# Optimization experiments

Measured on AMD Instinct MI355X. Metric: run time of the kernel, lower is better.

Reference implementation:

```python
import jax, jax.numpy as jnp
import numpy as np

N_NODES = 100000
N_EDGES = 1600000
IN_SIZE = 128
HIDDEN = 32
OUT_SIZE = 16


def _mean_agg(h, src, dst, n_nodes):
    # segment-sum of source features into destination nodes, then divide by in-degree
    summed = jax.ops.segment_sum(h[src], dst, num_segments=n_nodes)  # [N, D]
    deg = jax.ops.segment_sum(jnp.ones((src.shape[0],), h.dtype), dst, num_segments=n_nodes)
    return summed / jnp.maximum(deg, 1.0)[:, None]


def _sage_layer(h, src, dst, W_self, W_neigh, b):
    # DGL SAGEConv (mean): fc_self(h) + fc_neigh(mean_neigh(h)) + bias
    agg = _mean_agg(h, src, dst, h.shape[0])
    return h @ W_self + agg @ W_neigh + b


def setup_inputs() -> dict:
    key = jax.random.key(0)
    ks = jax.random.split(key, 9)
    inp = {
        "x": jax.random.normal(ks[0], (N_NODES, IN_SIZE), jnp.float32),
        "edge_src": jax.random.randint(ks[1], (N_EDGES,), 0, N_NODES, jnp.int32),
        "edge_dst": jax.random.randint(ks[2], (N_EDGES,), 0, N_NODES, jnp.int32),
        "W_self1": jax.random.normal(ks[3], (IN_SIZE, HIDDEN), jnp.float32) / np.sqrt(IN_SIZE),
        "W_neigh1": jax.random.normal(ks[4], (IN_SIZE, HIDDEN), jnp.float32) / np.sqrt(IN_SIZE),
        "b1": jnp.zeros((HIDDEN,), jnp.float32),
        "W_self2": jax.random.normal(ks[5], (HIDDEN, HIDDEN), jnp.float32) / np.sqrt(HIDDEN),
        "W_neigh2": jax.random.normal(ks[6], (HIDDEN, HIDDEN), jnp.float32) / np.sqrt(HIDDEN),
        "b2": jnp.zeros((HIDDEN,), jnp.float32),
        "W_self3": jax.random.normal(ks[7], (HIDDEN, OUT_SIZE), jnp.float32) / np.sqrt(HIDDEN),
        "W_neigh3": jax.random.normal(ks[8], (HIDDEN, OUT_SIZE), jnp.float32) / np.sqrt(HIDDEN),
        "b3": jnp.zeros((OUT_SIZE,), jnp.float32),
    }
    return inp


def reference(x, edge_src, edge_dst,
              W_self1, W_neigh1, b1,
              W_self2, W_neigh2, b2,
              W_self3, W_neigh3, b3):
    h = jax.nn.relu(_sage_layer(x, edge_src, edge_dst, W_self1, W_neigh1, b1))
    h = jax.nn.relu(_sage_layer(h, edge_src, edge_dst, W_self2, W_neigh2, b2))
    h = _sage_layer(h, edge_src, edge_dst, W_self3, W_neigh3, b3)
    return h
```

## Files before the change

kernel.cpp:

```cpp
#include <hip/hip_runtime.h>


#define BLOCK 256
#define NBLK 256
#define BSH 9
#define CAP 12288

typedef __attribute__((ext_vector_type(8))) short bf16x8;
typedef __attribute__((ext_vector_type(4))) float f32x4;

__device__ __forceinline__ unsigned pack_bf16(float a, float b) {
    unsigned ua = __float_as_uint(a); ua = (ua + 0x7fffu + ((ua >> 16) & 1u)) >> 16;
    unsigned ub = __float_as_uint(b); ub = (ub + 0x7fffu + ((ub >> 16) & 1u)) >> 16;
    return ua | (ub << 16);
}
__device__ __forceinline__ unsigned short bf16r(float f) {
    unsigned u = __float_as_uint(f);
    return (unsigned short)((u + 0x7fffu + ((u >> 16) & 1u)) >> 16);
}
__device__ __forceinline__ float bf2f(unsigned short u) {
    return __uint_as_float((unsigned)u << 16);
}

__global__ void prep_kernel(const float* __restrict__ Ws1, const float* __restrict__ Wn1,
                            const float* __restrict__ Ws2, const float* __restrict__ Wn2,
                            const float* __restrict__ Ws3, const float* __restrict__ Wn3,
                            unsigned short* __restrict__ Wt1,
                            unsigned short* __restrict__ Wt2,
                            unsigned short* __restrict__ Wt3) {
    int stride = gridDim.x * BLOCK;
    int t0 = blockIdx.x * BLOCK + threadIdx.x;
    for (int i = t0; i < 64 * 128; i += stride) {
        int o = i / 128, k = i % 128;
        float v = (o < 32) ? Ws1[k * 32 + o] : Wn1[k * 32 + (o - 32)];
        Wt1[i] = bf16r(v);
    }
    for (int i = t0; i < 64 * 32; i += stride) {
        int o = i / 32, k = i % 32;
        float v = (o < 32) ? Ws2[k * 32 + o] : Wn2[k * 32 + (o - 32)];
        Wt2[i] = bf16r(v);
    }
    for (int i = t0; i < 32 * 32; i += stride) {
        int o = i / 32, k = i % 32;
        float v = (o < 16) ? Ws3[k * 16 + o] : Wn3[k * 16 + (o - 16)];
        Wt3[i] = bf16r(v);
    }
}

__global__ __launch_bounds__(256, 4)
void stage1_kernel(const int* __restrict__ dst, int* __restrict__ hist,
                   int n_edges, int nbuk, int ch,
                   const float* __restrict__ x,
                   const unsigned short* __restrict__ Wt,
                   const float* __restrict__ bias,
                   unsigned short* __restrict__ pre,
                   unsigned short* __restrict__ p,
                   int n_nodes, int nHist) {
    __shared__ int cnt[256];
    int bid = blockIdx.x;
    int tid = threadIdx.x;

    if (bid < nHist) {
        for (int i = tid; i < nbuk; i += BLOCK) cnt[i] = 0;
        __syncthreads();
        int e0 = bid * ch;
        int e1 = e0 + ch; if (e1 > n_edges) e1 = n_edges;
        for (int e = e0 + tid; e < e1; e += BLOCK)
            atomicAdd(&cnt[dst[e] >> BSH], 1);
        __syncthreads();
        for (int i = tid; i < nbuk; i += BLOCK)
            hist[i * NBLK + bid] = cnt[i];
        return;
    }

    int pb = bid - nHist;
    int wv = tid >> 6, l = tid & 63;
    int col = l & 15, kg = l >> 4;
    int node0 = pb * 64 + wv * 16;

    int arow = node0 + col;
    if (arow >= n_nodes) arow = n_nodes - 1;
    const float* xr = x + (size_t)arow * 128 + kg * 8;

    f32x4 acc[4];
#pragma unroll
    for (int t = 0; t < 4; ++t) acc[t] = (f32x4){0.f, 0.f, 0.f, 0.f};

#pragma unroll
    for (int ks = 0; ks < 4; ++ks) {
        float4 f0 = *reinterpret_cast<const float4*>(xr + ks * 32);
        float4 f1 = *reinterpret_cast<const float4*>(xr + ks * 32 + 4);
        union { bf16x8 v; unsigned u[4]; } A;
        A.u[0] = pack_bf16(f0.x, f0.y);
        A.u[1] = pack_bf16(f0.z, f0.w);
        A.u[2] = pack_bf16(f1.x, f1.y);
        A.u[3] = pack_bf16(f1.z, f1.w);
#pragma unroll
        for (int t = 0; t < 4; ++t) {
            bf16x8 B = *reinterpret_cast<const bf16x8*>(
                Wt + (size_t)(t * 16 + col) * 128 + ks * 32 + kg * 8);
            acc[t] = __builtin_amdgcn_mfma_f32_16x16x32_bf16(A.v, B, acc[t], 0, 0, 0);
        }
    }

    int nodeb = node0 + kg * 4;
#pragma unroll
    for (int t = 0; t < 4; ++t) {
        int out = t * 16 + col;
#pragma unroll
        for (int r = 0; r < 4; ++r) {
            int node = nodeb + r;
            if (node >= n_nodes) continue;
            if (t < 2) {
                pre[(size_t)node * 32 + out] = bf16r(acc[t][r] + bias[out]);
            } else {
                p[(size_t)node * 32 + (out - 32)] = bf16r(acc[t][r]);
            }
        }
    }
}

__global__ void scanBlk_kernel(int* __restrict__ hist, int* __restrict__ buktot) {
    int b = blockIdx.x;
    int tid = threadIdx.x;
    int orig = hist[b * NBLK + tid];
    int v = orig;
    int lane = tid & 63, w = tid >> 6;
#pragma unroll
    for (int off = 1; off < 64; off <<= 1) {
        int u = __shfl_up(v, off);
        if (lane >= off) v += u;
    }
    __shared__ int wps[4];
    if (lane == 63) wps[w] = v;
    __syncthreads();
    int wadd = 0;
    for (int k = 0; k < w; ++k) wadd += wps[k];
    int excl = v - orig + wadd;
    hist[b * NBLK + tid] = excl;
    if (tid == 255) buktot[b] = excl + orig;
}

__global__ void scanBuk_kernel(const int* __restrict__ buktot, int* __restrict__ bukoff,
                               int nbuk, int* __restrict__ startp, int n_nodes, int n_edges) {
    int tid = threadIdx.x;
    int orig = (tid < nbuk) ? buktot[tid] : 0;
    int v = orig;
    int lane = tid & 63, w = tid >> 6;
#pragma unroll
    for (int off = 1; off < 64; off <<= 1) {
        int u = __shfl_up(v, off);
        if (lane >= off) v += u;
    }
    __shared__ int wps[4];
    if (lane == 63) wps[w] = v;
    __syncthreads();
    int wadd = 0;
    for (int k = 0; k < w; ++k) wadd += wps[k];
    int excl = v - orig + wadd;
    if (tid < nbuk) bukoff[tid] = excl;
    if (tid == 0) { bukoff[nbuk] = n_edges; startp[n_nodes] = n_edges; }
}

__global__ void part_kernel(const int* __restrict__ src, const int* __restrict__ dst,
                            const int* __restrict__ hist, const int* __restrict__ bukoff,
                            unsigned* __restrict__ pairs, int n_edges, int nbuk, int ch) {
    __shared__ int base[256];
    __shared__ int cnt[256];
    int tid = threadIdx.x;
    for (int i = tid; i < nbuk; i += BLOCK) {
        base[i] = hist[i * NBLK + blockIdx.x] + bukoff[i];
        cnt[i] = 0;
    }
    __syncthreads();
    int e0 = blockIdx.x * ch;
    int e1 = e0 + ch; if (e1 > n_edges) e1 = n_edges;
    for (int e = e0 + tid; e < e1; e += BLOCK) {
        int d = dst[e];
        int b = d >> BSH;
        unsigned dl = (unsigned)(d & ((1 << BSH) - 1));
        int r = atomicAdd(&cnt[b], 1);
        pairs[base[b] + r] = (unsigned)src[e] | (dl << 20);
    }
}

__global__ void build_kernel(const unsigned* __restrict__ pairs, const int* __restrict__ bukoff,
                             int* __restrict__ start, float* __restrict__ invdeg,
                             int* __restrict__ csr_src, int n_nodes) {
    __shared__ int deg[512];
    __shared__ int lst[512];
    __shared__ int cur[512];
    __shared__ int wps[4];
    __shared__ int scsr[CAP];

    int b = blockIdx.x;
    int tid = threadIdx.x;
    int e0 = bukoff[b];
    int e1 = bukoff[b + 1];
    int lo = b << BSH;
    int hi = lo + (1 << BSH); if (hi > n_nodes) hi = n_nodes;
    int nn = hi - lo;
    int ne = e1 - e0;

    for (int i = tid; i < 512; i += BLOCK) deg[i] = 0;
    __syncthreads();
    for (int i = e0 + tid; i < e1; i += BLOCK)
        atomicAdd(&deg[pairs[i] >> 20], 1);
    __syncthreads();

    int d0 = deg[2 * tid], d1 = deg[2 * tid + 1];
    int s = d0 + d1;
    int lane = tid & 63, w = tid >> 6;
    int v = s;
#pragma unroll
    for (int off = 1; off < 64; off <<= 1) {
        int u = __shfl_up(v, off);
        if (lane >= off) v += u;
    }
    if (lane == 63) wps[w] = v;
    __syncthreads();
    int wb = 0;
    for (int k = 0; k < w; ++k) wb += wps[k];
    int excl = wb + v - s;
    lst[2 * tid] = excl;
    lst[2 * tid + 1] = excl + d0;
    cur[2 * tid] = 0;
    cur[2 * tid + 1] = 0;
    __syncthreads();

    for (int i = tid; i < nn; i += BLOCK) {
        start[lo + i] = e0 + lst[i];
        int d = deg[i];
        invdeg[lo + i] = 1.0f / (float)(d < 1 ? 1 : d);
    }

    if (ne <= CAP) {
        for (int i = e0 + tid; i < e1; i += BLOCK) {
            unsigned pr = pairs[i];
            int dl = pr >> 20;
            int sl = lst[dl] + atomicAdd(&cur[dl], 1);
            scsr[sl] = (int)(pr & 0xFFFFFu);
        }
        __syncthreads();
        for (int i = tid; i < ne; i += BLOCK) csr_src[e0 + i] = scsr[i];
    } else {
        for (int i = e0 + tid; i < e1; i += BLOCK) {
            unsigned pr = pairs[i];
            int dl = pr >> 20;
            int sl = lst[dl] + atomicAdd(&cur[dl], 1);
            csr_src[e0 + sl] = (int)(pr & 0xFFFFFu);
        }
    }
}

template<int DOUT>
__global__ __launch_bounds__(256, 4)
void proj23_mfma(const unsigned short* __restrict__ h,
                 const unsigned short* __restrict__ Wt,
                 const float* __restrict__ bias,
                 unsigned short* __restrict__ pre,
                 unsigned short* __restrict__ p,
                 int n_nodes) {
    constexpr int NTILE = DOUT / 8;
    int tid = threadIdx.x;
    int wv = tid >> 6, l = tid & 63;
    int col = l & 15, kg = l >> 4;
    int node0 = blockIdx.x * 64 + wv * 16;

    int arow = node0 + col;
    if (arow >= n_nodes) arow = n_nodes - 1;
    bf16x8 A = *reinterpret_cast<const bf16x8*>(h + (size_t)arow * 32 + kg * 8);

    f32x4 acc[NTILE];
#pragma unroll
    for (int t = 0; t < NTILE; ++t) acc[t] = (f32x4){0.f, 0.f, 0.f, 0.f};

#pragma unroll
    for (int t = 0; t < NTILE; ++t) {
        bf16x8 B = *reinterpret_cast<const bf16x8*>(
            Wt + (size_t)(t * 16 + col) * 32 + kg * 8);
        acc[t] = __builtin_amdgcn_mfma_f32_16x16x32_bf16(A, B, acc[t], 0, 0, 0);
    }

    int nodeb = node0 + kg * 4;
#pragma unroll
    for (int t = 0; t < NTILE; ++t) {
        int out = t * 16 + col;
#pragma unroll
        for (int r = 0; r < 4; ++r) {
            int node = nodeb + r;
            if (node >= n_nodes) continue;
            if (out < DOUT) {
                pre[(size_t)node * DOUT + out] = bf16r(acc[t][r] + bias[out]);
            } else {
                p[(size_t)node * DOUT + (out - DOUT)] = bf16r(acc[t][r]);
            }
        }
    }
}

template<int D, bool RELU, bool BF16OUT>
__global__ void gather_kernel(const unsigned short* __restrict__ p,
                              const int* __restrict__ csr_src,
                              const int* __restrict__ start,
                              const unsigned short* __restrict__ pre,
                              const float* __restrict__ invdeg,
                              void* __restrict__ outv,
                              int n_nodes) {
    constexpr int NPW = 64 / D;
    int wave = threadIdx.x >> 6;
    int lane = threadIdx.x & 63;
    int g = (blockIdx.x * (blockDim.x >> 6) + wave) * NPW + lane / D;
    int f = lane % D;
    if (g >= n_nodes) return;
    int s0 = start[g];
    int s1 = start[g + 1];
    float a0 = 0.f, a1 = 0.f, a2 = 0.f, a3 = 0.f;
    float a4 = 0.f, a5 = 0.f, a6 = 0.f, a7 = 0.f;
    int j = s0;
    for (; j + 16 <= s1; j += 16) {
        int c[16];
#pragma unroll
        for (int q = 0; q < 16; ++q) c[q] = csr_src[j + q];
        unsigned short u[16];
#pragma unroll
        for (int q = 0; q < 16; ++q) u[q] = p[(size_t)c[q] * D + f];
        a0 += bf2f(u[0]) + bf2f(u[8]);
        a1 += bf2f(u[1]) + bf2f(u[9]);
        a2 += bf2f(u[2]) + bf2f(u[10]);
        a3 += bf2f(u[3]) + bf2f(u[11]);
        a4 += bf2f(u[4]) + bf2f(u[12]);
        a5 += bf2f(u[5]) + bf2f(u[13]);
        a6 += bf2f(u[6]) + bf2f(u[14]);
        a7 += bf2f(u[7]) + bf2f(u[15]);
    }
    for (; j + 4 <= s1; j += 4) {
        int c0 = csr_src[j], c1 = csr_src[j + 1];
        int c2 = csr_src[j + 2], c3 = csr_src[j + 3];
        a0 += bf2f(p[(size_t)c0 * D + f]);
        a1 += bf2f(p[(size_t)c1 * D + f]);
        a2 += bf2f(p[(size_t)c2 * D + f]);
        a3 += bf2f(p[(size_t)c3 * D + f]);
    }
    for (; j < s1; ++j)
        a4 += bf2f(p[(size_t)csr_src[j] * D + f]);
    float a = ((a0 + a1) + (a2 + a3)) + ((a4 + a5) + (a6 + a7));
    size_t o = (size_t)g * D + f;
    float v = bf2f(pre[o]) + a * invdeg[g];
    if (RELU) v = fmaxf(v, 0.f);
    if (BF16OUT) {
        ((unsigned short*)outv)[o] = bf16r(v);
    } else {
        ((float*)outv)[o] = v;
    }
}

extern "C" void kernel_launch(void* const* d_in, const int* in_sizes, int n_in,
                              void* d_out, int out_size, void* d_ws, size_t ws_size,
                              hipStream_t stream) {
    const float* x        = (const float*)d_in[0];
    const int*   edge_src = (const int*)d_in[1];
    const int*   edge_dst = (const int*)d_in[2];
    const float* Ws1 = (const float*)d_in[3];
    const float* Wn1 = (const float*)d_in[4];
    const float* b1  = (const float*)d_in[5];
    const float* Ws2 = (const float*)d_in[6];
    const float* Wn2 = (const float*)d_in[7];
    const float* b2  = (const float*)d_in[8];
    const float* Ws3 = (const float*)d_in[9];
    const float* Wn3 = (const float*)d_in[10];
    const float* b3  = (const float*)d_in[11];
    float* out = (float*)d_out;

    const int IN = 128, HID = 32;
    const int n_nodes = in_sizes[0] / IN;
    const int n_edges = in_sizes[1];
    const int nbuk = (n_nodes + (1 << BSH) - 1) >> BSH;
    const int ch   = (n_edges + NBLK - 1) / NBLK;

    char* wsb = (char*)d_ws;
    size_t off = 0;
    auto alloc = [&](size_t bytes) { char* r = wsb + off; off = (off + bytes + 255) & ~(size_t)255; return r; };
    int*   startp = (int*)alloc(((size_t)n_nodes + 1) * sizeof(int));
    float* invdeg = (float*)alloc((size_t)n_nodes * sizeof(float));
    int*   csr    = (int*)alloc((size_t)n_edges * sizeof(int));
    int*   hist   = (int*)alloc((size_t)nbuk * NBLK * sizeof(int));
    int*   buktot = (int*)alloc(256 * sizeof(int));
    int*   bukoff = (int*)alloc(257 * sizeof(int));
    unsigned short* Wt1 = (unsigned short*)alloc(64 * 128 * 2);
    unsigned short* Wt2 = (unsigned short*)alloc(64 * 32 * 2);
    unsigned short* Wt3 = (unsigned short*)alloc(32 * 32 * 2);
    unsigned* pairs = (unsigned*)alloc((size_t)n_edges * sizeof(unsigned));
    unsigned short* B0 = (unsigned short*)alloc((size_t)n_nodes * HID * 2);
    unsigned short* B1 = (unsigned short*)alloc((size_t)n_nodes * HID * 2);
    unsigned short* B3 = (unsigned short*)alloc((size_t)n_nodes * HID * 2);

    const int gP     = (n_nodes + 63) / 64;
    const int gGat32 = (n_nodes + 7) / 8;
    const int gGat16 = (n_nodes + 15) / 16;

    prep_kernel  <<<64, BLOCK, 0, stream>>>(Ws1, Wn1, Ws2, Wn2, Ws3, Wn3, Wt1, Wt2, Wt3);
    stage1_kernel<<<NBLK + gP, BLOCK, 0, stream>>>(edge_dst, hist, n_edges, nbuk, ch,
                                                   x, Wt1, b1, B0, B1, n_nodes, NBLK);
    scanBlk_kernel<<<nbuk, BLOCK, 0, stream>>>(hist, buktot);
    scanBuk_kernel<<<1, BLOCK, 0, stream>>>(buktot, bukoff, nbuk, startp, n_nodes, n_edges);
    part_kernel   <<<NBLK, BLOCK, 0, stream>>>(edge_src, edge_dst, hist, bukoff, pairs, n_edges, nbuk, ch);
    build_kernel  <<<nbuk, BLOCK, 0, stream>>>(pairs, bukoff, startp, invdeg, csr, n_nodes);

    gather_kernel<32, true, true><<<gGat32, BLOCK, 0, stream>>>(B1, csr, startp, B0, invdeg, B3, n_nodes);

    proj23_mfma<32><<<gP, BLOCK, 0, stream>>>(B3, Wt2, b2, B0, B1, n_nodes);
    gather_kernel<32, true, true><<<gGat32, BLOCK, 0, stream>>>(B1, csr, startp, B0, invdeg, B3, n_nodes);

    proj23_mfma<16><<<gP, BLOCK, 0, stream>>>(B3, Wt3, b3, B0, B1, n_nodes);
    gather_kernel<16, false, false><<<gGat16, BLOCK, 0, stream>>>(B1, csr, startp, B0, invdeg, out, n_nodes);
}
```

Measured before the change: 188.0 us.

## Fuse gather aggregation with next-layer MFMA projection via shared memory

Each 32-wide gather kernel is merged with the following layer's projection. A block of 16 nodes aggregates neighbours, applies ReLU, stores the bf16 hidden row in LDS, and then runs one 16x16x32 MFMA per output tile. This removes the intermediate hidden-state round trip through global memory and two kernel launches, and uses ping-pong C0/C1 buffers to avoid read/write aliasing. In exchange each block covers only 16 nodes and needs a __syncthreads, and some waves sit idle during the MFMA phase (only 2 tiles when DNEXT is 16).

Measured after the change: 182.0 us (median of 2 runs). 1.03x faster.

```diff
diff --git a/kernel.cpp b/kernel.cpp
--- a/kernel.cpp
+++ b/kernel.cpp
@@ -253,60 +253,104 @@
     }
 }
 
-template<int DOUT>
-__global__ __launch_bounds__(256, 4)
-void proj23_mfma(const unsigned short* __restrict__ h,
+template<int DNEXT>
+__global__ __launch_bounds__(256, 8)
+void gather_proj(const unsigned short* __restrict__ p,
+                 const int* __restrict__ csr_src,
+                 const int* __restrict__ start,
+                 const unsigned short* __restrict__ pre,
+                 const float* __restrict__ invdeg,
                  const unsigned short* __restrict__ Wt,
                  const float* __restrict__ bias,
-                 unsigned short* __restrict__ pre,
-                 unsigned short* __restrict__ p,
+                 unsigned short* __restrict__ pre_out,
+                 unsigned short* __restrict__ p_out,
                  int n_nodes) {
-    constexpr int NTILE = DOUT / 8;
-    int tid = threadIdx.x;
-    int wv = tid >> 6, l = tid & 63;
-    int col = l & 15, kg = l >> 4;
-    int node0 = blockIdx.x * 64 + wv * 16;
-
-    int arow = node0 + col;
-    if (arow >= n_nodes) arow = n_nodes - 1;
-    bf16x8 A = *reinterpret_cast<const bf16x8*>(h + (size_t)arow * 32 + kg * 8);
-
-    f32x4 acc[NTILE];
-#pragma unroll
-    for (int t = 0; t < NTILE; ++t) acc[t] = (f32x4){0.f, 0.f, 0.f, 0.f};
-
-#pragma unroll
-    for (int t = 0; t < NTILE; ++t) {
-        bf16x8 B = *reinterpret_cast<const bf16x8*>(
-            Wt + (size_t)(t * 16 + col) * 32 + kg * 8);
-        acc[t] = __builtin_amdgcn_mfma_f32_16x16x32_bf16(A, B, acc[t], 0, 0, 0);
-    }
-
-    int nodeb = node0 + kg * 4;
-#pragma unroll
-    for (int t = 0; t < NTILE; ++t) {
-        int out = t * 16 + col;
-#pragma unroll
-        for (int r = 0; r < 4; ++r) {
-            int node = nodeb + r;
-            if (node >= n_nodes) continue;
-            if (out < DOUT) {
-                pre[(size_t)node * DOUT + out] = bf16r(acc[t][r] + bias[out]);
-            } else {
-                p[(size_t)node * DOUT + (out - DOUT)] = bf16r(acc[t][r]);
+    constexpr int NTILE = 2 * DNEXT / 16;
+    __shared__ unsigned short sh[16][32];
+
+    int tid = threadIdx.x;
+    int wv = tid >> 6, lane = tid & 63;
+    int base = blockIdx.x * 16;
+    int f = lane & 31;
+
+#pragma unroll
+    for (int it = 0; it < 2; ++it) {
+        int nl = wv * 4 + it * 2 + (lane >> 5);
+        int g = base + nl;
+        float v = 0.f;
+        if (g < n_nodes) {
+            int s0 = start[g];
+            int s1 = start[g + 1];
+            float a0 = 0.f, a1 = 0.f, a2 = 0.f, a3 = 0.f;
+            float a4 = 0.f, a5 = 0.f, a6 = 0.f, a7 = 0.f;
+            int j = s0;
+            for (; j + 16 <= s1; j += 16) {
+                int c[16];
+#pragma unroll
+                for (int q = 0; q < 16; ++q) c[q] = csr_src[j + q];
+                unsigned short u[16];
+#pragma unroll
+                for (int q = 0; q < 16; ++q) u[q] = p[(size_t)c[q] * 32 + f];
+                a0 += bf2f(u[0]) + bf2f(u[8]);
+                a1 += bf2f(u[1]) + bf2f(u[9]);
+                a2 += bf2f(u[2]) + bf2f(u[10]);
+                a3 += bf2f(u[3]) + bf2f(u[11]);
+                a4 += bf2f(u[4]) + bf2f(u[12]);
+                a5 += bf2f(u[5]) + bf2f(u[13]);
+                a6 += bf2f(u[6]) + bf2f(u[14]);
+                a7 += bf2f(u[7]) + bf2f(u[15]);
             }
-        }
-    }
-}
-
-template<int D, bool RELU, bool BF16OUT>
-__global__ void gather_kernel(const unsigned short* __restrict__ p,
-                              const int* __restrict__ csr_src,
-                              const int* __restrict__ start,
-                              const unsigned short* __restrict__ pre,
-                              const float* __restrict__ invdeg,
-                              void* __restrict__ outv,
-                              int n_nodes) {
+            for (; j + 4 <= s1; j += 4) {
+                int c0 = csr_src[j], c1 = csr_src[j + 1];
+                int c2 = csr_src[j + 2], c3 = csr_src[j + 3];
+                a0 += bf2f(p[(size_t)c0 * 32 + f]);
+                a1 += bf2f(p[(size_t)c1 * 32 + f]);
+                a2 += bf2f(p[(size_t)c2 * 32 + f]);
+                a3 += bf2f(p[(size_t)c3 * 32 + f]);
+            }
+            for (; j < s1; ++j)
+                a4 += bf2f(p[(size_t)csr_src[j] * 32 + f]);
+            float a = ((a0 + a1) + (a2 + a3)) + ((a4 + a5) + (a6 + a7));
+            size_t o = (size_t)g * 32 + f;
+            v = bf2f(pre[o]) + a * invdeg[g];
+            v = fmaxf(v, 0.f);
+        }
+        sh[nl][f] = bf16r(v);
+    }
+    __syncthreads();
+
+    int t = wv;
+    if (t >= NTILE) return;
+    int col = lane & 15, kg = lane >> 4;
+
+    bf16x8 A = *reinterpret_cast<const bf16x8*>(&sh[col][kg * 8]);
+    bf16x8 B = *reinterpret_cast<const bf16x8*>(
+        Wt + (size_t)(t * 16 + col) * 32 + kg * 8);
+    f32x4 acc = (f32x4){0.f, 0.f, 0.f, 0.f};
+    acc = __builtin_amdgcn_mfma_f32_16x16x32_bf16(A, B, acc, 0, 0, 0);
+
+    int out = t * 16 + col;
+    int nodeb = base + kg * 4;
+#pragma unroll
+    for (int r = 0; r < 4; ++r) {
+        int node = nodeb + r;
+        if (node >= n_nodes) continue;
+        if (out < DNEXT) {
+            pre_out[(size_t)node * DNEXT + out] = bf16r(acc[r] + bias[out]);
+        } else {
+            p_out[(size_t)node * DNEXT + (out - DNEXT)] = bf16r(acc[r]);
+        }
+    }
+}
+
+__global__ void gather_final(const unsigned short* __restrict__ p,
+                             const int* __restrict__ csr_src,
+                             const int* __restrict__ start,
+                             const unsigned short* __restrict__ pre,
+                             const float* __restrict__ invdeg,
+                             float* __restrict__ out,
+                             int n_nodes) {
+    constexpr int D = 16;
     constexpr int NPW = 64 / D;
     int wave = threadIdx.x >> 6;
     int lane = threadIdx.x & 63;
@@ -346,13 +390,7 @@
         a4 += bf2f(p[(size_t)csr_src[j] * D + f]);
     float a = ((a0 + a1) + (a2 + a3)) + ((a4 + a5) + (a6 + a7));
     size_t o = (size_t)g * D + f;
-    float v = bf2f(pre[o]) + a * invdeg[g];
-    if (RELU) v = fmaxf(v, 0.f);
-    if (BF16OUT) {
-        ((unsigned short*)outv)[o] = bf16r(v);
-    } else {
-        ((float*)outv)[o] = v;
-    }
+    out[o] = bf2f(pre[o]) + a * invdeg[g];
 }
 
 extern "C" void kernel_launch(void* const* d_in, const int* in_sizes, int n_in,
@@ -393,10 +431,11 @@
     unsigned* pairs = (unsigned*)alloc((size_t)n_edges * sizeof(unsigned));
     unsigned short* B0 = (unsigned short*)alloc((size_t)n_nodes * HID * 2);
     unsigned short* B1 = (unsigned short*)alloc((size_t)n_nodes * HID * 2);
-    unsigned short* B3 = (unsigned short*)alloc((size_t)n_nodes * HID * 2);
-
-    const int gP     = (n_nodes + 63) / 64;
-    const int gGat32 = (n_nodes + 7) / 8;
+    unsigned short* C0 = (unsigned short*)alloc((size_t)n_nodes * HID * 2);
+    unsigned short* C1 = (unsigned short*)alloc((size_t)n_nodes * HID * 2);
+
+    const int gP   = (n_nodes + 63) / 64;
+    const int gGP  = (n_nodes + 15) / 16;
     const int gGat16 = (n_nodes + 15) / 16;
 
     prep_kernel  <<<64, BLOCK, 0, stream>>>(Ws1, Wn1, Ws2, Wn2, Ws3, Wn3, Wt1, Wt2, Wt3);
@@ -407,11 +446,9 @@
     part_kernel   <<<NBLK, BLOCK, 0, stream>>>(edge_src, edge_dst, hist, bukoff, pairs, n_edges, nbuk, ch);
     build_kernel  <<<nbuk, BLOCK, 0, stream>>>(pairs, bukoff, startp, invdeg, csr, n_nodes);
 
-    gather_kernel<32, true, true><<<gGat32, BLOCK, 0, stream>>>(B1, csr, startp, B0, invdeg, B3, n_nodes);
-
-    proj23_mfma<32><<<gP, BLOCK, 0, stream>>>(B3, Wt2, b2, B0, B1, n_nodes);
-    gather_kernel<32, true, true><<<gGat32, BLOCK, 0, stream>>>(B1, csr, startp, B0, invdeg, B3, n_nodes);
-
-    proj23_mfma<16><<<gP, BLOCK, 0, stream>>>(B3, Wt3, b3, B0, B1, n_nodes);
-    gather_kernel<16, false, false><<<gGat16, BLOCK, 0, stream>>>(B1, csr, startp, B0, invdeg, out, n_nodes);
-}
+    gather_proj<32><<<gGP, BLOCK, 0, stream>>>(B1, csr, startp, B0, invdeg, Wt2, b2, C0, C1, n_nodes);
+
+    gather_proj<16><<<gGP, BLOCK, 0, stream>>>(C1, csr, startp, C0, invdeg, Wt3, b3, B0, B1, n_nodes);
+
+    gather_final<<<gGat16, BLOCK, 0, stream>>>(B1, csr, startp, B0, invdeg, out, n_nodes);
+}
```
